# Kernel optimization log

Measured on AMD Instinct MI355X. Metric: run time of the kernel, lower is better.

## Reference

```python
import jax, jax.numpy as jnp
import numpy as np

C = 128   # channels / dim
NH = 4    # num heads
HD = C // NH
K = 5     # conv kernel size: t=int((log2(128)+1)/2)=4 -> k=5
P = 12    # patch size
GH = 8    # grid height/width (96/12)
NPATCH = GH * GH
FEAT = P * P * C


def _ln(x, g, b):
    m = jnp.mean(x, -1, keepdims=True)
    v = jnp.var(x, -1, keepdims=True)
    return (x - m) / jnp.sqrt(v + 1e-5) * g + b


def _conv1d(x, w, pad):
    return jax.lax.conv_general_dilated(x, w, (1,), [(pad, pad)], dimension_numbers=('NCH', 'OIH', 'NCH'))


def _pool(x, out):
    # exact adaptive avg pool when H % out == 0
    B, c, H, W = x.shape
    f = H // out
    return x.reshape(B, c, out, f, out, f).mean((3, 5))


def _bilinear_ac(x, out):
    # bilinear interpolate [B,C,H,H] -> [B,C,out,out], align_corners=True
    H = x.shape[2]
    cpos = jnp.arange(out) * (H - 1) / (out - 1)
    i0 = jnp.floor(cpos).astype(jnp.int32)
    i1 = jnp.minimum(i0 + 1, H - 1)
    w = (cpos - i0).astype(x.dtype)
    xh = x[:, :, i0, :] * (1 - w)[None, None, :, None] + x[:, :, i1, :] * w[None, None, :, None]
    return xh[:, :, :, i0] * (1 - w) + xh[:, :, :, i1] * w


def setup_inputs() -> dict:
    key = jax.random.key(0)
    ks = jax.random.split(key, 8)
    B = 16
    return {
        's1': jax.random.normal(ks[0], (B, C, 96, 96), jnp.float32),
        'o': jax.random.normal(ks[1], (B, C, 64, 64), jnp.float32),
        'index': jax.random.randint(ks[2], (4, 2), 0, 96),
        'pe_w': jax.random.normal(ks[3], (64, 64, K), jnp.float32) * 0.05,
        'bn_g': jnp.ones((64,), jnp.float32),
        'bn_b': jnp.zeros((64,), jnp.float32),
        'bn_m': jnp.zeros((64,), jnp.float32),
        'bn_v': jnp.ones((64,), jnp.float32),
        'lnx_g': jnp.ones((C,), jnp.float32),
        'lnx_b': jnp.zeros((C,), jnp.float32),
        'lny_g': jnp.ones((C,), jnp.float32),
        'lny_b': jnp.zeros((C,), jnp.float32),
        'qkv_w': jax.random.normal(ks[4], (3 * C, C), jnp.float32) * 0.02,
        'qkv_b': jnp.zeros((3 * C,), jnp.float32),
        'yv_w': jax.random.normal(ks[5], (C, C), jnp.float32) * 0.02,
        'yv_b': jnp.zeros((C,), jnp.float32),
        'proj_w': jax.random.normal(ks[6], (C, C), jnp.float32) * 0.02,
        'proj_b': jnp.zeros((C,), jnp.float32),
        'c1d_w': jax.random.normal(ks[7], (C, C, K), jnp.float32) * 0.05,
    }


def reference(s1, o, index, pe_w, bn_g, bn_b, bn_m, bn_v, lnx_g, lnx_b, lny_g, lny_b,
              qkv_w, qkv_b, yv_w, yv_b, proj_w, proj_b, c1d_w):
    B = s1.shape[0]
    pad = (K - 1) // 2
    # --- mask(s1): patch embedding, conv1d+BN(eval)+ReLU, selective-square mask ---
    # einops: b c (h p1) (w p2) -> b (h w) (p1 p2 c)
    x = s1.reshape(B, C, GH, P, GH, P).transpose(0, 2, 4, 3, 5, 1).reshape(B, NPATCH, FEAT)
    x = _conv1d(x, pe_w, pad)
    x = (x - bn_m[None, :, None]) / jnp.sqrt(bn_v + 1e-5)[None, :, None] * bn_g[None, :, None] + bn_b[None, :, None]
    x = jax.nn.relu(x)
    # mask: rows at center indices keep value (mul by 1), all other rows squared
    idxs = index[:, 0] // P * GH + index[:, 1] // P
    sel = jnp.zeros((NPATCH,), bool).at[idxs].set(True)
    x = x * jnp.where(sel[None, :, None], 1.0, x)
    # einops back: b (h w) (p1 p2 c) -> b c (h p1) (w p2), then pool to 32
    x = x.reshape(B, GH, GH, P, P, C).transpose(0, 5, 1, 3, 2, 4).reshape(B, C, 96, 96)
    short = _pool(x, 32)                                   # [B,C,32,32]
    # --- attention branch ---
    op = _pool(o, 32)
    N = 32 * 32
    of = _ln(op.reshape(B, C, N).transpose(0, 2, 1), lnx_g, lnx_b)   # [B,N,C]
    ori = short.reshape(B, C, N).transpose(0, 2, 1)
    sn = _ln(ori, lny_g, lny_b)
    qkv = (of @ qkv_w.T + qkv_b).reshape(B, N, 3, NH, HD).transpose(2, 0, 3, 1, 4)
    q, k, v = qkv[0], qkv[1], qkv[2]                       # each [B,H,N,D]
    yv = (sn @ yv_w.T + yv_b).reshape(B, N, NH, HD).transpose(0, 2, 1, 3)
    attn = jax.nn.softmax(jnp.einsum('bhnd,bhmd->bhnm', q, k) * HD ** -0.5, axis=-1)
    xv = v + jnp.einsum('bhnm,bhmd->bhnd', attn, yv)
    xv = xv.transpose(0, 2, 1, 3).reshape(B, N, C) @ proj_w.T + proj_b
    xv = (xv + ori).transpose(0, 2, 1)                     # [B,C,N]
    xv = xv + _conv1d(xv, c1d_w, pad)
    xv = xv.reshape(B, C, 32, 32)
    return _bilinear_ac(xv, 96)
```

## Files before the change

kernel.cpp:

```cpp
#include <hip/hip_runtime.h>

#define FEAT 18432

typedef __attribute__((ext_vector_type(8))) short short8;
typedef __attribute__((ext_vector_type(4))) float f32x4;

__device__ __forceinline__ float b2f(unsigned short s) {
  union { unsigned int u; float f; } v; v.u = ((unsigned int)s) << 16; return v.f;
}
__device__ __forceinline__ unsigned short f2bf(float x) {
  union { float f; unsigned int u; } v; v.f = x;
  unsigned int u = v.u;
  unsigned int r = (u + 0x7FFFu + ((u >> 16) & 1u)) >> 16;
  return (unsigned short)r;
}

__device__ __forceinline__ void gl_lds16(const void* g, void* l) {
  __builtin_amdgcn_global_load_lds(
      (const __attribute__((address_space(1))) unsigned int*)g,
      (__attribute__((address_space(3))) unsigned int*)l, 16, 0, 0);
}

__global__ __launch_bounds__(256) void k_transpose(const float* __restrict__ s1,
                                                   unsigned short* __restrict__ xT) {
  int c = blockIdx.x, b = blockIdx.y;
  __shared__ float lds[96 * 99];
  int t = threadIdx.x;
  const float* src = s1 + ((size_t)b * 128 + c) * 9216;
  for (int idx = t; idx < 2304; idx += 256) {
    float4 v = ((const float4*)src)[idx];
    int h = idx / 24, w0 = (idx - h * 24) * 4;
    float* p = lds + h * 99 + w0;
    p[0] = v.x; p[1] = v.y; p[2] = v.z; p[3] = v.w;
  }
  __syncthreads();
  unsigned short* dstb = xT + (size_t)b * FEAT * 64;
  int sw = c & 7;
  for (int idx = t; idx < 1152; idx += 256) {
    int p1p2 = idx >> 3, gh = idx & 7;
    int p1 = p1p2 / 12, p2 = p1p2 - p1 * 12;
    const float* row = lds + (gh * 12 + p1) * 99 + p2;
    uint4 u;
    u.x = f2bf(row[0])  | ((unsigned int)f2bf(row[12]) << 16);
    u.y = f2bf(row[24]) | ((unsigned int)f2bf(row[36]) << 16);
    u.z = f2bf(row[48]) | ((unsigned int)f2bf(row[60]) << 16);
    u.w = f2bf(row[72]) | ((unsigned int)f2bf(row[84]) << 16);
    int f = p1p2 * 128 + c;
    int pos = gh ^ sw;
    *(uint4*)(dstb + (size_t)f * 64 + pos * 8) = u;
  }
}

__global__ __launch_bounds__(256) void k_prep(const float* __restrict__ pe_w,
                                              unsigned short* __restrict__ wpk) {
  int oc0 = blockIdx.x * 8;
  for (int e = threadIdx.x; e < 2560; e += 256) {
    int oc = oc0 + e / 320;
    int kL = e - (e / 320) * 320;
    int ic = kL & 63, kk = kL >> 6;
    float v = pe_w[(oc * 64 + ic) * 5 + kk];
    int LC = kL >> 3;
    int pos = (LC & 56) | ((LC & 7) ^ (oc & 7));
    wpk[oc * 320 + (pos << 3) + (kL & 7)] = f2bf(v);
  }
}

__global__ __launch_bounds__(256) void k_prepc(const float* __restrict__ cw,
                                               float* __restrict__ cwt) {
  int e0 = (blockIdx.x * 256 + threadIdx.x) * 4;
#pragma unroll
  for (int j = 0; j < 4; ++j) {
    int e = e0 + j;
    int r = e >> 7, oc = e & 127;
    cwt[e] = cw[(size_t)oc * 640 + r];
  }
}

__global__ __launch_bounds__(256) void k_prepw(const float* __restrict__ W,
                                               unsigned short* __restrict__ dst,
                                               int ncols) {
  int idx = blockIdx.x * 256 + threadIdx.x;
  if (idx >= ncols * 16) return;
  int n = idx >> 4, c = idx & 15;
  int slot = (c & 8) | ((c & 7) ^ (n & 7));
  const float* s = W + (size_t)n * 128 + c * 8;
  uint4 u;
  u.x = (unsigned int)f2bf(s[0]) | ((unsigned int)f2bf(s[1]) << 16);
  u.y = (unsigned int)f2bf(s[2]) | ((unsigned int)f2bf(s[3]) << 16);
  u.z = (unsigned int)f2bf(s[4]) | ((unsigned int)f2bf(s[5]) << 16);
  u.w = (unsigned int)f2bf(s[6]) | ((unsigned int)f2bf(s[7]) << 16);
  *(uint4*)(dst + (size_t)n * 128 + slot * 8) = u;
}

__global__ __launch_bounds__(256) void k_conv_pe(
    const unsigned short* __restrict__ xT, const unsigned short* __restrict__ wpk,
    const float* __restrict__ bn_g, const float* __restrict__ bn_b,
    const float* __restrict__ bn_m, const float* __restrict__ bn_v,
    const int* __restrict__ indexp, unsigned short* __restrict__ ym) {
  extern __shared__ char smem[];
  unsigned short* Wl = (unsigned short*)smem;
  unsigned short* xl = (unsigned short*)(smem + 40960);
  float* scf = (float*)(smem + 74240);
  float* shf = (float*)(smem + 74496);
  int*   sli = (int*)(smem + 74752);
  int t = threadIdx.x;
  int b = blockIdx.y;
  int blk_f0 = blockIdx.x << 9;
  int lane = t & 63, w = t >> 6;
  int n16 = lane & 15, q = lane >> 4;

  for (int j = 0; j < 10; ++j) {
    int seg = w * 10 + j;
    gl_lds16((const char*)wpk + (seg << 10) + lane * 16, (char*)Wl + (seg << 10));
  }
  if (t < 64) {
    float sc = bn_g[t] * rsqrtf(bn_v[t] + 1e-5f);
    scf[t] = sc;
    shf[t] = bn_b[t] - bn_m[t] * sc;
    int i0 = indexp[0] / 12 * 8 + indexp[1] / 12;
    int i1 = indexp[2] / 12 * 8 + indexp[3] / 12;
    int i2 = indexp[4] / 12 * 8 + indexp[5] / 12;
    int i3 = indexp[6] / 12 * 8 + indexp[7] / 12;
    sli[t] = (t == i0 || t == i1 || t == i2 || t == i3) ? 1 : 0;
  }

  const unsigned short* xb = xT + (size_t)b * FEAT * 64;
  const unsigned int* xbu = (const unsigned int*)xb;

  for (int wnd = 0; wnd < 2; ++wnd) {
    int F0 = blk_f0 + (wnd << 8);
    __syncthreads();
    int flA = (F0 == 0) ? 2 : 0;
    for (int j = 0; j < 8; ++j) {
      int seg = (w << 3) + j;
      int gRow = F0 - 2 + flA + (seg << 3);
      gl_lds16((const char*)xb + (size_t)gRow * 128 + lane * 16,
               (char*)xl + flA * 128 + (seg << 10));
    }
    if (t < 128) {
      int r0 = (flA == 2) ? 0 : 256;
      int fl = (t < 64) ? (r0 + (t >> 5)) : (258 + ((t >> 5) & 1));
      int j = t & 31;
      int f = F0 - 2 + fl;
      unsigned int v = 0;
      if (f >= 0 && f < FEAT) v = xbu[(size_t)f * 32 + j];
      ((unsigned int*)xl)[fl * 32 + j] = v;
    }
    __syncthreads();

    f32x4 acc[4][4];
#pragma unroll
    for (int mt = 0; mt < 4; ++mt)
#pragma unroll
      for (int nt = 0; nt < 4; ++nt) acc[mt][nt] = (f32x4){0.f, 0.f, 0.f, 0.f};

    int rowB = w * 64 + n16;
#pragma unroll
    for (int kk = 0; kk < 5; ++kk) {
      int swb = (n16 + kk + 6) & 7;
#pragma unroll
      for (int ih = 0; ih < 2; ++ih) {
        int ca = (ih << 2) | q;
        const unsigned short* Ap = Wl + kk * 64 + ((ca ^ (n16 & 7)) << 3) + n16 * 320;
        short8 a0 = *(const short8*)(Ap);
        short8 a1 = *(const short8*)(Ap + 16 * 320);
        short8 a2 = *(const short8*)(Ap + 32 * 320);
        short8 a3 = *(const short8*)(Ap + 48 * 320);
        const unsigned short* Bp = xl + ((ca ^ swb) << 3) + (rowB + kk) * 64;
        short8 b0 = *(const short8*)(Bp);
        short8 b1 = *(const short8*)(Bp + 16 * 64);
        short8 b2 = *(const short8*)(Bp + 32 * 64);
        short8 b3 = *(const short8*)(Bp + 48 * 64);
        acc[0][0] = __builtin_amdgcn_mfma_f32_16x16x32_bf16(a0, b0, acc[0][0], 0, 0, 0);
        acc[0][1] = __builtin_amdgcn_mfma_f32_16x16x32_bf16(a0, b1, acc[0][1], 0, 0, 0);
        acc[0][2] = __builtin_amdgcn_mfma_f32_16x16x32_bf16(a0, b2, acc[0][2], 0, 0, 0);
        acc[0][3] = __builtin_amdgcn_mfma_f32_16x16x32_bf16(a0, b3, acc[0][3], 0, 0, 0);
        acc[1][0] = __builtin_amdgcn_mfma_f32_16x16x32_bf16(a1, b0, acc[1][0], 0, 0, 0);
        acc[1][1] = __builtin_amdgcn_mfma_f32_16x16x32_bf16(a1, b1, acc[1][1], 0, 0, 0);
        acc[1][2] = __builtin_amdgcn_mfma_f32_16x16x32_bf16(a1, b2, acc[1][2], 0, 0, 0);
        acc[1][3] = __builtin_amdgcn_mfma_f32_16x16x32_bf16(a1, b3, acc[1][3], 0, 0, 0);
        acc[2][0] = __builtin_amdgcn_mfma_f32_16x16x32_bf16(a2, b0, acc[2][0], 0, 0, 0);
        acc[2][1] = __builtin_amdgcn_mfma_f32_16x16x32_bf16(a2, b1, acc[2][1], 0, 0, 0);
        acc[2][2] = __builtin_amdgcn_mfma_f32_16x16x32_bf16(a2, b2, acc[2][2], 0, 0, 0);
        acc[2][3] = __builtin_amdgcn_mfma_f32_16x16x32_bf16(a2, b3, acc[2][3], 0, 0, 0);
        acc[3][0] = __builtin_amdgcn_mfma_f32_16x16x32_bf16(a3, b0, acc[3][0], 0, 0, 0);
        acc[3][1] = __builtin_amdgcn_mfma_f32_16x16x32_bf16(a3, b1, acc[3][1], 0, 0, 0);
        acc[3][2] = __builtin_amdgcn_mfma_f32_16x16x32_bf16(a3, b2, acc[3][2], 0, 0, 0);
        acc[3][3] = __builtin_amdgcn_mfma_f32_16x16x32_bf16(a3, b3, acc[3][3], 0, 0, 0);
      }
    }

#pragma unroll
    for (int mt = 0; mt < 4; ++mt) {
#pragma unroll
      for (int i = 0; i < 4; ++i) {
        int oc = mt * 16 + q * 4 + i;
        float sc = scf[oc], sh = shf[oc];
        bool sel = sli[oc] != 0;
        unsigned short* yo = ym + ((size_t)b * 64 + oc) * FEAT + F0 + w * 64 + n16;
#pragma unroll
        for (int nt = 0; nt < 4; ++nt) {
          float y = fmaf(acc[mt][nt][i], sc, sh);
          y = fmaxf(y, 0.f);
          if (!sel) y *= y;
          yo[nt * 16] = f2bf(y);
        }
      }
    }
  }
}

__global__ __launch_bounds__(256) void k_pool9ln(
    const unsigned short* __restrict__ ym, const float* __restrict__ lng,
    const float* __restrict__ lnb, float* __restrict__ ori,
    unsigned short* __restrict__ snh) {
  int oc = blockIdx.x, b = blockIdx.y;
  const unsigned short* src = ym + ((size_t)b * 64 + oc) * FEAT;
  int oh0 = (oc >> 3) << 2, ow0 = (oc & 7) << 2;
  __shared__ float red[8];
  int t = threadIdx.x;
  int c = t & 127, hr = t >> 7, wv = t >> 6, l64 = t & 63;
  float g = lng[c], bb = lnb[c];
  for (int p = 0; p < 8; ++p) {
    int nl = p * 2 + hr;
    int pg1 = nl >> 2, pg2 = nl & 3;
    int pbase = (pg1 * 36 + pg2 * 3) * 128 + c;
    float s = 0.f;
#pragma unroll
    for (int dy = 0; dy < 3; ++dy)
#pragma unroll
      for (int dx = 0; dx < 3; ++dx)
        s += b2f(src[pbase + (dy * 12 + dx) * 128]);
    float val = s * (1.f / 9.f);
    float su = val, q = val * val;
#pragma unroll
    for (int off = 32; off > 0; off >>= 1) {
      su += __shfl_xor(su, off, 64);
      q += __shfl_xor(q, off, 64);
    }
    if (l64 == 0) { red[wv * 2] = su; red[wv * 2 + 1] = q; }
    __syncthreads();
    float S = red[hr * 4 + 0] + red[hr * 4 + 2];
    float Q = red[hr * 4 + 1] + red[hr * 4 + 3];
    float mean = S * (1.f / 128.f);
    float var = Q * (1.f / 128.f) - mean * mean;
    float inv = rsqrtf(var + 1e-5f);
    int n = (oh0 + pg1) * 32 + ow0 + pg2;
    size_t base = ((size_t)b * 1024 + n) * 128;
    ori[base + c] = val;
    float lnv = (val - mean) * inv * g + bb;
    int ch = c >> 3;
    int slot = (ch & 8) | ((ch & 7) ^ (n & 7));
    snh[base + slot * 8 + (c & 7)] = f2bf(lnv);
    __syncthreads();
  }
}

__global__ __launch_bounds__(256) void k_poolo_ln(
    const float* __restrict__ o, const float* __restrict__ lng,
    const float* __restrict__ lnb, unsigned short* __restrict__ oflh) {
  int y = blockIdx.x, b = blockIdx.y;
  __shared__ float pl[128 * 33];
  int t = threadIdx.x;
  for (int idx = t; idx < 4096; idx += 256) {
    int xo = idx & 31, c = idx >> 5;
    const float* p = o + (((size_t)b * 128 + c) * 64 + 2 * y) * 64 + 2 * xo;
    float2 a = *(const float2*)p;
    float2 d = *(const float2*)(p + 64);
    pl[c * 33 + xo] = 0.25f * (a.x + a.y + d.x + d.y);
  }
  __syncthreads();
  int xo = t >> 3, l8 = t & 7;
  float v[16]; float s = 0.f, q = 0.f;
#pragma unroll
  for (int i = 0; i < 16; ++i) {
    float x = pl[(l8 * 16 + i) * 33 + xo];
    v[i] = x; s += x; q += x * x;
  }
#pragma unroll
  for (int off = 1; off < 8; off <<= 1) {
    s += __shfl_xor(s, off, 8);
    q += __shfl_xor(q, off, 8);
  }
  float mean = s * (1.f / 128.f);
  float var = q * (1.f / 128.f) - mean * mean;
  float inv = rsqrtf(var + 1e-5f);
  int n = y * 32 + xo;
  unsigned short* dst = oflh + ((size_t)b * 1024 + n) * 128;
  int m7 = n & 7;
#pragma unroll
  for (int h = 0; h < 2; ++h) {
    int c = l8 * 2 + h;
    int slot = (c & 8) | ((c & 7) ^ m7);
    uint4 u;
    float w0 = (v[h * 8 + 0] - mean) * inv * lng[c * 8 + 0] + lnb[c * 8 + 0];
    float w1 = (v[h * 8 + 1] - mean) * inv * lng[c * 8 + 1] + lnb[c * 8 + 1];
    float w2 = (v[h * 8 + 2] - mean) * inv * lng[c * 8 + 2] + lnb[c * 8 + 2];
    float w3 = (v[h * 8 + 3] - mean) * inv * lng[c * 8 + 3] + lnb[c * 8 + 3];
    float w4 = (v[h * 8 + 4] - mean) * inv * lng[c * 8 + 4] + lnb[c * 8 + 4];
    float w5 = (v[h * 8 + 5] - mean) * inv * lng[c * 8 + 5] + lnb[c * 8 + 5];
    float w6 = (v[h * 8 + 6] - mean) * inv * lng[c * 8 + 6] + lnb[c * 8 + 6];
    float w7 = (v[h * 8 + 7] - mean) * inv * lng[c * 8 + 7] + lnb[c * 8 + 7];
    u.x = (unsigned int)f2bf(w0) | ((unsigned int)f2bf(w1) << 16);
    u.y = (unsigned int)f2bf(w2) | ((unsigned int)f2bf(w3) << 16);
    u.z = (unsigned int)f2bf(w4) | ((unsigned int)f2bf(w5) << 16);
    u.w = (unsigned int)f2bf(w6) | ((unsigned int)f2bf(w7) << 16);
    *(uint4*)(dst + slot * 8) = u;
  }
}

__global__ __launch_bounds__(256) void k_gemm_mfma(
    const unsigned short* __restrict__ A, const unsigned short* __restrict__ W,
    const float* __restrict__ bias, float* __restrict__ out, int Ncols) {
  __shared__ unsigned short Al[128 * 128];
  __shared__ unsigned short Bl[64 * 128];
  int m0 = blockIdx.x << 7, n0 = blockIdx.y << 6;
  int t = threadIdx.x;
  int lane = t & 63, w = t >> 6;
  int n16 = lane & 15, q = lane >> 4;

  for (int j = 0; j < 8; ++j) {
    int seg = w * 8 + j;
    gl_lds16((const char*)A + (size_t)m0 * 256 + (seg << 10) + lane * 16,
             (char*)Al + (seg << 10));
  }
  for (int j = 0; j < 4; ++j) {
    int seg = w * 4 + j;
    gl_lds16((const char*)W + (size_t)n0 * 256 + (seg << 10) + lane * 16,
             (char*)Bl + (seg << 10));
  }
  __syncthreads();

  int wm = w >> 1, wn = w & 1;
  f32x4 acc[4][2];
#pragma unroll
  for (int mt = 0; mt < 4; ++mt)
#pragma unroll
    for (int nt = 0; nt < 2; ++nt) acc[mt][nt] = (f32x4){0.f, 0.f, 0.f, 0.f};

#pragma unroll
  for (int kf = 0; kf < 4; ++kf) {
    int ca = kf * 4 + q;
    int rA0 = wm * 64 + n16;
    const unsigned short* Ap0 = Al + (size_t)rA0 * 128;
    int slotA = (ca & 8) | ((ca & 7) ^ (rA0 & 7));
    short8 a0 = *(const short8*)(Ap0 + slotA * 8);
    short8 a1 = *(const short8*)(Ap0 + 16 * 128 + slotA * 8);
    short8 a2 = *(const short8*)(Ap0 + 32 * 128 + slotA * 8);
    short8 a3 = *(const short8*)(Ap0 + 48 * 128 + slotA * 8);
    int rB0 = wn * 32 + n16;
    const unsigned short* Bp0 = Bl + (size_t)rB0 * 128;
    int slotB = (ca & 8) | ((ca & 7) ^ (rB0 & 7));
    short8 b0 = *(const short8*)(Bp0 + slotB * 8);
    short8 b1 = *(const short8*)(Bp0 + 16 * 128 + slotB * 8);
    acc[0][0] = __builtin_amdgcn_mfma_f32_16x16x32_bf16(a0, b0, acc[0][0], 0, 0, 0);
    acc[0][1] = __builtin_amdgcn_mfma_f32_16x16x32_bf16(a0, b1, acc[0][1], 0, 0, 0);
    acc[1][0] = __builtin_amdgcn_mfma_f32_16x16x32_bf16(a1, b0, acc[1][0], 0, 0, 0);
    acc[1][1] = __builtin_amdgcn_mfma_f32_16x16x32_bf16(a1, b1, acc[1][1], 0, 0, 0);
    acc[2][0] = __builtin_amdgcn_mfma_f32_16x16x32_bf16(a2, b0, acc[2][0], 0, 0, 0);
    acc[2][1] = __builtin_amdgcn_mfma_f32_16x16x32_bf16(a2, b1, acc[2][1], 0, 0, 0);
    acc[3][0] = __builtin_amdgcn_mfma_f32_16x16x32_bf16(a3, b0, acc[3][0], 0, 0, 0);
    acc[3][1] = __builtin_amdgcn_mfma_f32_16x16x32_bf16(a3, b1, acc[3][1], 0, 0, 0);
  }

#pragma unroll
  for (int mt = 0; mt < 4; ++mt) {
#pragma unroll
    for (int i = 0; i < 4; ++i) {
      int m = m0 + wm * 64 + mt * 16 + q * 4 + i;
#pragma unroll
      for (int nt = 0; nt < 2; ++nt) {
        int n = n0 + wn * 32 + nt * 16 + n16;
        out[(size_t)m * Ncols + n] = acc[mt][nt][i] + bias[n];
      }
    }
  }
}

__global__ __launch_bounds__(256) void k_proj_mfma(
    const unsigned short* __restrict__ A, const unsigned short* __restrict__ W,
    const float* __restrict__ bias, const float* __restrict__ ori,
    float* __restrict__ xv2) {
  __shared__ unsigned short Al[128 * 128];
  __shared__ unsigned short Bl[64 * 128];
  int m0 = blockIdx.x << 7, n0 = blockIdx.y << 6;
  int t = threadIdx.x;
  int lane = t & 63, w = t >> 6;
  int n16 = lane & 15, q = lane >> 4;

  for (int j = 0; j < 8; ++j) {
    int seg = w * 8 + j;
    gl_lds16((const char*)A + (size_t)m0 * 256 + (seg << 10) + lane * 16,
             (char*)Al + (seg << 10));
  }
  for (int j = 0; j < 4; ++j) {
    int seg = w * 4 + j;
    gl_lds16((const char*)W + (size_t)n0 * 256 + (seg << 10) + lane * 16,
             (char*)Bl + (seg << 10));
  }
  __syncthreads();

  int wm = w >> 1, wn = w & 1;
  f32x4 acc[4][2];
#pragma unroll
  for (int mt = 0; mt < 4; ++mt)
#pragma unroll
    for (int nt = 0; nt < 2; ++nt) acc[mt][nt] = (f32x4){0.f, 0.f, 0.f, 0.f};

#pragma unroll
  for (int kf = 0; kf < 4; ++kf) {
    int ca = kf * 4 + q;
    int rA0 = wm * 64 + n16;
    const unsigned short* Ap0 = Al + (size_t)rA0 * 128;
    int slotA = (ca & 8) | ((ca & 7) ^ (rA0 & 7));
    short8 a0 = *(const short8*)(Ap0 + slotA * 8);
    short8 a1 = *(const short8*)(Ap0 + 16 * 128 + slotA * 8);
    short8 a2 = *(const short8*)(Ap0 + 32 * 128 + slotA * 8);
    short8 a3 = *(const short8*)(Ap0 + 48 * 128 + slotA * 8);
    int rB0 = wn * 32 + n16;
    const unsigned short* Bp0 = Bl + (size_t)rB0 * 128;
    int slotB = (ca & 8) | ((ca & 7) ^ (rB0 & 7));
    short8 b0 = *(const short8*)(Bp0 + slotB * 8);
    short8 b1 = *(const short8*)(Bp0 + 16 * 128 + slotB * 8);
    acc[0][0] = __builtin_amdgcn_mfma_f32_16x16x32_bf16(a0, b0, acc[0][0], 0, 0, 0);
    acc[0][1] = __builtin_amdgcn_mfma_f32_16x16x32_bf16(a0, b1, acc[0][1], 0, 0, 0);
    acc[1][0] = __builtin_amdgcn_mfma_f32_16x16x32_bf16(a1, b0, acc[1][0], 0, 0, 0);
    acc[1][1] = __builtin_amdgcn_mfma_f32_16x16x32_bf16(a1, b1, acc[1][1], 0, 0, 0);
    acc[2][0] = __builtin_amdgcn_mfma_f32_16x16x32_bf16(a2, b0, acc[2][0], 0, 0, 0);
    acc[2][1] = __builtin_amdgcn_mfma_f32_16x16x32_bf16(a2, b1, acc[2][1], 0, 0, 0);
    acc[3][0] = __builtin_amdgcn_mfma_f32_16x16x32_bf16(a3, b0, acc[3][0], 0, 0, 0);
    acc[3][1] = __builtin_amdgcn_mfma_f32_16x16x32_bf16(a3, b1, acc[3][1], 0, 0, 0);
  }

  int bb = m0 >> 10;
  int nbase = (m0 & 1023) + wm * 64;
#pragma unroll
  for (int mt = 0; mt < 4; ++mt) {
    int nloc = nbase + mt * 16 + q * 4;
    const float* orow = ori + ((size_t)bb * 1024 + nloc) * 128;
#pragma unroll
    for (int nt = 0; nt < 2; ++nt) {
      int c = n0 + wn * 32 + nt * 16 + n16;
      float pb = bias[c];
      float4 vv;
      vv.x = acc[mt][nt][0] + pb + orow[c];
      vv.y = acc[mt][nt][1] + pb + orow[128 + c];
      vv.z = acc[mt][nt][2] + pb + orow[256 + c];
      vv.w = acc[mt][nt][3] + pb + orow[384 + c];
      *(float4*)(xv2 + ((size_t)bb * 128 + c) * 1024 + nloc) = vv;
    }
  }
}

__global__ __launch_bounds__(256) void k_cvt(const float* __restrict__ qkv,
                                             const float* __restrict__ yv,
                                             unsigned short* __restrict__ qkb,
                                             unsigned short* __restrict__ vtb) {
  int nt = blockIdx.x, b = blockIdx.y;
  int n0 = nt << 6;
  int t = threadIdx.x;
  __shared__ unsigned short tl[64 * 132];
  const float* qb = qkv + ((size_t)b * 1024 + n0) * 384;
  for (int it = 0; it < 16; ++it) {
    int idx = it * 256 + t;
    int n = idx >> 6, c4 = idx & 63;
    float4 v = *(const float4*)(qb + (size_t)n * 384 + c4 * 4);
    int c = c4 << 2;
    int kind = c >> 7, h = (c >> 5) & 3, d = c & 31;
    uint2 u;
    u.x = (unsigned int)f2bf(v.x) | ((unsigned int)f2bf(v.y) << 16);
    u.y = (unsigned int)f2bf(v.z) | ((unsigned int)f2bf(v.w) << 16);
    *(uint2*)(qkb + ((((size_t)b * 4 + h) * 2 + kind) * 1024 + n0 + n) * 32 + d) = u;
  }
  const float* vb = yv + ((size_t)b * 1024 + n0) * 128;
  for (int it = 0; it < 8; ++it) {
    int idx = it * 256 + t;
    int n = idx >> 5, c4 = idx & 31;
    float4 v = *(const float4*)(vb + (size_t)n * 128 + c4 * 4);
    unsigned short* o = tl + n * 132 + c4 * 4;
    o[0] = f2bf(v.x); o[1] = f2bf(v.y); o[2] = f2bf(v.z); o[3] = f2bf(v.w);
  }
  __syncthreads();
  int c = t >> 1, half = t & 1;
  unsigned short* orow = vtb + (((size_t)b * 4 + (c >> 5)) * 32 + (c & 31)) * 1024 + n0 + half * 32;
#pragma unroll
  for (int k = 0; k < 4; ++k) {
    short8 pack;
#pragma unroll
    for (int j = 0; j < 8; ++j)
      pack[j] = (short)tl[(half * 32 + k * 8 + j) * 132 + c];
    *(short8*)(orow + k * 8) = pack;
  }
}

__global__ __launch_bounds__(256) void k_attn(const float* __restrict__ qkv,
                                              const unsigned short* __restrict__ qkb,
                                              const unsigned short* __restrict__ vtb,
                                              unsigned short* __restrict__ atth) {
  int qt = blockIdx.x, h = blockIdx.y, b = blockIdx.z;
  __shared__ unsigned short Qs[64 * 40];
  __shared__ unsigned short Ks[64 * 40];
  __shared__ unsigned short Vt[32 * 72];
  __shared__ unsigned short Pw[4 * 16 * 68];
  int t = threadIdx.x;
  int lane = t & 63, w = t >> 6;
  int quad = lane >> 4, l16 = lane & 15;
  const float* qbase = qkv + (size_t)b * 1024 * 384;
  const unsigned short* qrow = qkb + (((size_t)b * 4 + h) * 2 + 0) * 1024 * 32;
  const unsigned short* krow = qkb + (((size_t)b * 4 + h) * 2 + 1) * 1024 * 32;
  const unsigned short* vrow = vtb + ((size_t)b * 4 + h) * 32 * 1024;
  int q0 = qt << 6;
  int hd = h * 32;

  {
    int r = t >> 2, cq = t & 3;
    short8 v = *(const short8*)(qrow + (size_t)(q0 + r) * 32 + cq * 8);
    *(short8*)(Qs + r * 40 + cq * 8) = v;
  }
  __syncthreads();
  short8 aq = *(const short8*)(Qs + (w * 16 + l16) * 40 + quad * 8);

  f32x4 O[2];
  O[0] = (f32x4){0.f, 0.f, 0.f, 0.f};
  O[1] = (f32x4){0.f, 0.f, 0.f, 0.f};
  float mi0 = -1e30f, li0 = 0.f;
  unsigned short* Pme = Pw + w * (16 * 68);
  const float scl = 0.17677669529663688f;

  for (int ci = 0; ci < 16; ++ci) {
    __syncthreads();
    int kn0 = ci << 6;
    {
      int r = t >> 2, cq = t & 3;
      short8 kv = *(const short8*)(krow + (size_t)(kn0 + r) * 32 + cq * 8);
      *(short8*)(Ks + r * 40 + cq * 8) = kv;
      int d = t >> 3, cc = t & 7;
      short8 vv = *(const short8*)(vrow + (size_t)d * 1024 + kn0 + cc * 8);
      *(short8*)(Vt + d * 72 + cc * 8) = vv;
    }
    __syncthreads();

    f32x4 S[4];
#pragma unroll
    for (int nt = 0; nt < 4; ++nt) S[nt] = (f32x4){0.f, 0.f, 0.f, 0.f};
#pragma unroll
    for (int nt = 0; nt < 4; ++nt) {
      short8 bk = *(const short8*)(Ks + (nt * 16 + l16) * 40 + quad * 8);
      S[nt] = __builtin_amdgcn_mfma_f32_16x16x32_bf16(bk, aq, S[nt], 0, 0, 0);
    }

    float sv[16];
#pragma unroll
    for (int nt = 0; nt < 4; ++nt)
#pragma unroll
      for (int r = 0; r < 4; ++r) sv[nt * 4 + r] = S[nt][r] * scl;
    float m0 = fmaxf(fmaxf(sv[0], sv[1]), fmaxf(sv[2], sv[3]));
    float m1 = fmaxf(fmaxf(sv[4], sv[5]), fmaxf(sv[6], sv[7]));
    float m2 = fmaxf(fmaxf(sv[8], sv[9]), fmaxf(sv[10], sv[11]));
    float m3 = fmaxf(fmaxf(sv[12], sv[13]), fmaxf(sv[14], sv[15]));
    float rm = fmaxf(fmaxf(m0, m1), fmaxf(m2, m3));
    rm = fmaxf(rm, __shfl_xor(rm, 16));
    rm = fmaxf(rm, __shfl_xor(rm, 32));
    float nm = fmaxf(mi0, rm);
    float alpha = __expf(mi0 - nm);
    mi0 = nm;

    float psnt[4];
    unsigned short* pwr = Pme + l16 * 68 + quad * 4;
#pragma unroll
    for (int nt = 0; nt < 4; ++nt) {
      float p0 = __expf(sv[nt * 4 + 0] - nm);
      float p1 = __expf(sv[nt * 4 + 1] - nm);
      float p2 = __expf(sv[nt * 4 + 2] - nm);
      float p3 = __expf(sv[nt * 4 + 3] - nm);
      psnt[nt] = (p0 + p1) + (p2 + p3);
      uint2 u;
      u.x = (unsigned int)f2bf(p0) | ((unsigned int)f2bf(p1) << 16);
      u.y = (unsigned int)f2bf(p2) | ((unsigned int)f2bf(p3) << 16);
      *(uint2*)(pwr + nt * 16) = u;
    }
    float ps = (psnt[0] + psnt[1]) + (psnt[2] + psnt[3]);
    ps += __shfl_xor(ps, 16);
    ps += __shfl_xor(ps, 32);
    li0 = li0 * alpha + ps;

    float al0 = __shfl(alpha, quad * 4 + 0);
    float al1 = __shfl(alpha, quad * 4 + 1);
    float al2 = __shfl(alpha, quad * 4 + 2);
    float al3 = __shfl(alpha, quad * 4 + 3);
    O[0][0] *= al0; O[1][0] *= al0;
    O[0][1] *= al1; O[1][1] *= al1;
    O[0][2] *= al2; O[1][2] *= al2;
    O[0][3] *= al3; O[1][3] *= al3;

#pragma unroll
    for (int kc = 0; kc < 2; ++kc) {
      short8 bv0 = *(const short8*)(Vt + l16 * 72 + kc * 32 + quad * 8);
      short8 bv1 = *(const short8*)(Vt + (16 + l16) * 72 + kc * 32 + quad * 8);
      short8 ap = *(const short8*)(Pme + l16 * 68 + kc * 32 + quad * 8);
      O[0] = __builtin_amdgcn_mfma_f32_16x16x32_bf16(ap, bv0, O[0], 0, 0, 0);
      O[1] = __builtin_amdgcn_mfma_f32_16x16x32_bf16(ap, bv1, O[1], 0, 0, 0);
    }
  }

#pragma unroll
  for (int reg = 0; reg < 4; ++reg) {
    float lit = __shfl(li0, quad * 4 + reg);
    int n = q0 + w * 16 + quad * 4 + reg;
    float inv = 1.f / lit;
    size_t mrow = ((size_t)b * 1024 + n) * 128;
    int m7 = n & 7;
#pragma unroll
    for (int nt = 0; nt < 2; ++nt) {
      int dd = hd + nt * 16 + l16;
      float val = O[nt][reg] * inv + qbase[(size_t)n * 384 + 256 + dd];
      int ch = dd >> 3;
      int slot = (ch & 8) | ((ch & 7) ^ m7);
      atth[mrow + slot * 8 + (dd & 7)] = f2bf(val);
    }
  }
}

__global__ __launch_bounds__(256) void k_conv1d(
    const float* __restrict__ xv2, const float* __restrict__ cwt,
    float* __restrict__ xv3) {
  extern __shared__ char cs[];
  float* xl = (float*)cs;
  float* wl = (float*)(cs + 18432);
  int nt = blockIdx.x, b = blockIdx.y;
  int n0 = nt << 5;
  int t = threadIdx.x;
  int lane = t & 63, w = t >> 6;
  const float* xb = xv2 + (size_t)b * 128 * 1024;
  for (int idx = t; idx < 4608; idx += 256) {
    int ic = idx / 36, j = idx - ic * 36;
    int n = n0 + j - 2;
    xl[idx] = (n >= 0 && n < 1024) ? xb[(size_t)ic * 1024 + n] : 0.f;
  }

  int oc = t & 127, g = t >> 7;
  float acc[16];
#pragma unroll
  for (int i = 0; i < 16; ++i) acc[i] = 0.f;

#pragma unroll 1
  for (int ch = 0; ch < 16; ++ch) {
    __syncthreads();
#pragma unroll
    for (int j = 0; j < 5; ++j) {
      int seg = w * 5 + j;
      gl_lds16((const char*)cwt + (size_t)ch * 20480 + (seg << 10) + lane * 16,
               (char*)wl + (seg << 10));
    }
    __syncthreads();

#pragma unroll
    for (int icl = 0; icl < 8; ++icl) {
      int ic = ch * 8 + icl;
      const float* xr = xl + ic * 36 + (g << 4);
      float xw[20];
#pragma unroll
      for (int q2 = 0; q2 < 5; ++q2) {
        float4 v = *(const float4*)(xr + q2 * 4);
        xw[q2 * 4] = v.x; xw[q2 * 4 + 1] = v.y; xw[q2 * 4 + 2] = v.z; xw[q2 * 4 + 3] = v.w;
      }
      const float* wr = wl + icl * 5 * 128 + oc;
      float w0 = wr[0], w1 = wr[128], w2 = wr[256], w3 = wr[384], w4 = wr[512];
#pragma unroll
      for (int i = 0; i < 16; ++i)
        acc[i] = fmaf(xw[i], w0, fmaf(xw[i + 1], w1, fmaf(xw[i + 2], w2,
                 fmaf(xw[i + 3], w3, fmaf(xw[i + 4], w4, acc[i])))));
    }
  }

  const float* res = xb + (size_t)oc * 1024 + n0 + (g << 4);
  float* outp = xv3 + ((size_t)b * 128 + oc) * 1024 + n0 + (g << 4);
#pragma unroll
  for (int q2 = 0; q2 < 4; ++q2) {
    float4 r = *(const float4*)(res + q2 * 4);
    float4 o_;
    o_.x = r.x + acc[q2 * 4 + 0];
    o_.y = r.y + acc[q2 * 4 + 1];
    o_.z = r.z + acc[q2 * 4 + 2];
    o_.w = r.w + acc[q2 * 4 + 3];
    *(float4*)(outp + q2 * 4) = o_;
  }
}

__global__ __launch_bounds__(256) void k_bilinear(const float* __restrict__ xv3,
                                                  float* __restrict__ out) {
  int idx = blockIdx.x * 256 + threadIdx.x;
  int X = idx % 96;
  int t2 = idx / 96;
  int Y = t2 % 96;
  int bc = t2 / 96;
  const float* src = xv3 + (size_t)bc * 1024;
  const float r = 31.f / 95.f;
  float py = Y * r, px = X * r;
  int y0 = (int)py, x0 = (int)px;
  float wy = py - y0, wx = px - x0;
  int y1 = y0 < 31 ? y0 + 1 : 31, x1 = x0 < 31 ? x0 + 1 : 31;
  float a = src[y0 * 32 + x0], b_ = src[y0 * 32 + x1];
  float c_ = src[y1 * 32 + x0], d_ = src[y1 * 32 + x1];
  float t0 = a * (1.f - wy) + c_ * wy;
  float t1 = b_ * (1.f - wy) + d_ * wy;
  out[idx] = t0 * (1.f - wx) + t1 * wx;
}

extern "C" void kernel_launch(void* const* d_in, const int* in_sizes, int n_in,
                              void* d_out, int out_size, void* d_ws, size_t ws_size,
                              hipStream_t stream) {
  (void)in_sizes; (void)n_in; (void)out_size; (void)ws_size;
  const float* s1    = (const float*)d_in[0];
  const float* o     = (const float*)d_in[1];
  const int*   indx  = (const int*)d_in[2];
  const float* pe_w  = (const float*)d_in[3];
  const float* bn_g  = (const float*)d_in[4];
  const float* bn_b  = (const float*)d_in[5];
  const float* bn_m  = (const float*)d_in[6];
  const float* bn_v  = (const float*)d_in[7];
  const float* lnx_g = (const float*)d_in[8];
  const float* lnx_b = (const float*)d_in[9];
  const float* lny_g = (const float*)d_in[10];
  const float* lny_b = (const float*)d_in[11];
  const float* qkv_w = (const float*)d_in[12];
  const float* qkv_b = (const float*)d_in[13];
  const float* yv_w  = (const float*)d_in[14];
  const float* yv_b  = (const float*)d_in[15];
  const float* proj_w = (const float*)d_in[16];
  const float* proj_b = (const float*)d_in[17];
  const float* c1d_w  = (const float*)d_in[18];

  char* ws = (char*)d_ws;
  unsigned short* xTh = (unsigned short*)ws;
  unsigned short* ymh = (unsigned short*)(ws + 37748736);
  unsigned short* wpk = (unsigned short*)d_out;
  float* cwt = (float*)((char*)d_out + 65536);
  unsigned short* wqkh = (unsigned short*)((char*)d_out + 458752);
  unsigned short* wyvh = (unsigned short*)((char*)d_out + 573440);
  unsigned short* wprh = (unsigned short*)((char*)d_out + 622592);
  float* ori  = (float*)ws;
  unsigned short* snh  = (unsigned short*)(ws + 8388608);
  unsigned short* oflh = (unsigned short*)(ws + 16777216);
  unsigned short* atth = (unsigned short*)(ws + 25165824);
  float* qkvb  = (float*)(ws + 37748736);
  float* yvbuf = (float*)(ws + 62914560);
  unsigned short* qkb = (unsigned short*)(ws + 16777216);
  unsigned short* vtb = (unsigned short*)(ws + 71303168);
  float* xv2   = (float*)(ws + 37748736);
  float* xv3   = (float*)(ws + 46137344);

  hipLaunchKernelGGL(k_prep, dim3(8), dim3(256), 0, stream, pe_w, wpk);
  hipLaunchKernelGGL(k_prepc, dim3(80), dim3(256), 0, stream, c1d_w, cwt);
  hipLaunchKernelGGL(k_prepw, dim3(24), dim3(256), 0, stream, qkv_w, wqkh, 384);
  hipLaunchKernelGGL(k_prepw, dim3(8), dim3(256), 0, stream, yv_w, wyvh, 128);
  hipLaunchKernelGGL(k_prepw, dim3(8), dim3(256), 0, stream, proj_w, wprh, 128);
  hipLaunchKernelGGL(k_transpose, dim3(128, 16), dim3(256), 0, stream, s1, xTh);
  hipLaunchKernelGGL(k_conv_pe, dim3(36, 16), dim3(256), 75008, stream,
                     xTh, wpk, bn_g, bn_b, bn_m, bn_v, indx, ymh);
  hipLaunchKernelGGL(k_pool9ln, dim3(64, 16), dim3(256), 0, stream, ymh, lny_g, lny_b, ori, snh);
  hipLaunchKernelGGL(k_poolo_ln, dim3(32, 16), dim3(256), 0, stream, o, lnx_g, lnx_b, oflh);
  hipLaunchKernelGGL(k_gemm_mfma, dim3(128, 6), dim3(256), 0, stream, oflh, wqkh, qkv_b, qkvb, 384);
  hipLaunchKernelGGL(k_gemm_mfma, dim3(128, 2), dim3(256), 0, stream, snh, wyvh, yv_b, yvbuf, 128);
  hipLaunchKernelGGL(k_cvt, dim3(16, 16), dim3(256), 0, stream, qkvb, yvbuf, qkb, vtb);
  hipLaunchKernelGGL(k_attn, dim3(16, 4, 16), dim3(256), 0, stream, qkvb, qkb, vtb, atth);
  hipLaunchKernelGGL(k_proj_mfma, dim3(128, 2), dim3(256), 0, stream, atth, wprh, proj_b, ori, xv2);
  hipLaunchKernelGGL(k_conv1d, dim3(32, 16), dim3(256), 38912, stream, xv2, cwt, xv3);
  hipLaunchKernelGGL(k_bilinear, dim3(73728), dim3(256), 0, stream, xv3, (float*)d_out);
}
```

Before: 393.6 us.

## Run channel conv1d as bf16 MFMA GEMM with swizzled LDS tiles

Replaces the scalar FP32 conv1d over channels with an MFMA bf16 implicit GEMM. The weights are prepacked into a swizzled bf16 layout, and the projection kernel also emits a bf16 position-major copy of its output that serves as the conv input. The goal is to move the 128x640 per-position contraction off the FP32 FMA pipes onto matrix cores. In exchange it adds an extra bf16 write in proj and uses bf16 precision for the conv operands.

```diff
diff --git a/kernel.cpp b/kernel.cpp
--- a/kernel.cpp
+++ b/kernel.cpp
@@ -65,15 +65,15 @@
   }
 }
 
-__global__ __launch_bounds__(256) void k_prepc(const float* __restrict__ cw,
-                                               float* __restrict__ cwt) {
-  int e0 = (blockIdx.x * 256 + threadIdx.x) * 4;
-#pragma unroll
-  for (int j = 0; j < 4; ++j) {
-    int e = e0 + j;
-    int r = e >> 7, oc = e & 127;
-    cwt[e] = cw[(size_t)oc * 640 + r];
-  }
+__global__ __launch_bounds__(256) void k_prepcw(const float* __restrict__ cw,
+                                                unsigned short* __restrict__ wch) {
+  int e = blockIdx.x * 256 + threadIdx.x;
+  int oc = e / 640, kl = e - (e / 640) * 640;
+  int kk = kl >> 7, ic = kl & 127;
+  float v = cw[(size_t)oc * 640 + ic * 5 + kk];
+  int LC = kl >> 3;
+  int pos = (LC & 120) | ((LC & 7) ^ (oc & 7));
+  wch[(size_t)oc * 640 + pos * 8 + (kl & 7)] = f2bf(v);
 }
 
 __global__ __launch_bounds__(256) void k_prepw(const float* __restrict__ W,
@@ -380,7 +380,7 @@
 __global__ __launch_bounds__(256) void k_proj_mfma(
     const unsigned short* __restrict__ A, const unsigned short* __restrict__ W,
     const float* __restrict__ bias, const float* __restrict__ ori,
-    float* __restrict__ xv2) {
+    float* __restrict__ xv2, unsigned short* __restrict__ xph) {
   __shared__ unsigned short Al[128 * 128];
   __shared__ unsigned short Bl[64 * 128];
   int m0 = blockIdx.x << 7, n0 = blockIdx.y << 6;
@@ -448,6 +448,14 @@
       vv.z = acc[mt][nt][2] + pb + orow[256 + c];
       vv.w = acc[mt][nt][3] + pb + orow[384 + c];
       *(float4*)(xv2 + ((size_t)bb * 128 + c) * 1024 + nloc) = vv;
+      int ch = c >> 3, ce = c & 7;
+#pragma unroll
+      for (int i = 0; i < 4; ++i) {
+        int nrow = nloc + i;
+        int slot = (ch & 8) | ((ch & 7) ^ (nrow & 7));
+        float val = (i == 0) ? vv.x : (i == 1) ? vv.y : (i == 2) ? vv.z : vv.w;
+        xph[((size_t)bb * 1024 + nrow) * 128 + slot * 8 + ce] = f2bf(val);
+      }
     }
   }
 }
@@ -621,69 +629,86 @@
   }
 }
 
-__global__ __launch_bounds__(256) void k_conv1d(
-    const float* __restrict__ xv2, const float* __restrict__ cwt,
-    float* __restrict__ xv3) {
+__global__ __launch_bounds__(256) void k_conv1d_mfma(
+    const unsigned short* __restrict__ xph, const unsigned short* __restrict__ wch,
+    const float* __restrict__ xv2, float* __restrict__ xv3) {
   extern __shared__ char cs[];
-  float* xl = (float*)cs;
-  float* wl = (float*)(cs + 18432);
-  int nt = blockIdx.x, b = blockIdx.y;
-  int n0 = nt << 5;
-  int t = threadIdx.x;
-  int lane = t & 63, w = t >> 6;
-  const float* xb = xv2 + (size_t)b * 128 * 1024;
-  for (int idx = t; idx < 4608; idx += 256) {
-    int ic = idx / 36, j = idx - ic * 36;
+  unsigned short* Wl = (unsigned short*)cs;
+  unsigned short* xl = (unsigned short*)(cs + 81920);
+  int ntile = blockIdx.x, b = blockIdx.y, oh = blockIdx.z;
+  int n0 = ntile << 7;
+  int t = threadIdx.x, lane = t & 63, w = t >> 6;
+  int n16 = lane & 15, q = lane >> 4;
+
+  const unsigned short* wsrc = wch + (size_t)oh * 64 * 640;
+  for (int j = 0; j < 20; ++j) {
+    int seg = w * 20 + j;
+    gl_lds16((const char*)wsrc + (seg << 10) + lane * 16, (char*)Wl + (seg << 10));
+  }
+  const unsigned short* xpb = xph + (size_t)b * 1024 * 128;
+  for (int j = 0; j < 8; ++j) {
+    int seg = w * 8 + j;
+    gl_lds16((const char*)xpb + (size_t)n0 * 256 + (seg << 10) + lane * 16,
+             (char*)xl + 512 + (seg << 10));
+  }
+  {
+    int ri = t >> 6, j2 = t & 63;
+    int j = (ri < 2) ? ri : (128 + ri);
     int n = n0 + j - 2;
-    xl[idx] = (n >= 0 && n < 1024) ? xb[(size_t)ic * 1024 + n] : 0.f;
-  }
-
-  int oc = t & 127, g = t >> 7;
-  float acc[16];
-#pragma unroll
-  for (int i = 0; i < 16; ++i) acc[i] = 0.f;
-
-#pragma unroll 1
-  for (int ch = 0; ch < 16; ++ch) {
-    __syncthreads();
-#pragma unroll
-    for (int j = 0; j < 5; ++j) {
-      int seg = w * 5 + j;
-      gl_lds16((const char*)cwt + (size_t)ch * 20480 + (seg << 10) + lane * 16,
-               (char*)wl + (seg << 10));
-    }
-    __syncthreads();
-
-#pragma unroll
-    for (int icl = 0; icl < 8; ++icl) {
-      int ic = ch * 8 + icl;
-      const float* xr = xl + ic * 36 + (g << 4);
-      float xw[20];
-#pragma unroll
-      for (int q2 = 0; q2 < 5; ++q2) {
-        float4 v = *(const float4*)(xr + q2 * 4);
-        xw[q2 * 4] = v.x; xw[q2 * 4 + 1] = v.y; xw[q2 * 4 + 2] = v.z; xw[q2 * 4 + 3] = v.w;
+    unsigned int v = 0;
+    if (n >= 0 && n < 1024) v = ((const unsigned int*)xpb)[(size_t)n * 64 + j2];
+    ((unsigned int*)xl)[j * 64 + j2] = v;
+  }
+  __syncthreads();
+
+  f32x4 acc[4][2];
+#pragma unroll
+  for (int mt = 0; mt < 4; ++mt)
+#pragma unroll
+    for (int nt = 0; nt < 2; ++nt) acc[mt][nt] = (f32x4){0.f, 0.f, 0.f, 0.f};
+
+  int nb = w * 32;
+#pragma unroll
+  for (int kk = 0; kk < 5; ++kk) {
+    int swb = (n16 + kk + 6) & 7;
+#pragma unroll
+    for (int kf = 0; kf < 4; ++kf) {
+      int ca = kf * 4 + q;
+      int LC = kk * 16 + kf * 4 + q;
+      int slotA = (LC & 120) | ((LC & 7) ^ (n16 & 7));
+      const unsigned short* Ap = Wl + n16 * 640 + slotA * 8;
+      short8 a0 = *(const short8*)(Ap);
+      short8 a1 = *(const short8*)(Ap + 16 * 640);
+      short8 a2 = *(const short8*)(Ap + 32 * 640);
+      short8 a3 = *(const short8*)(Ap + 48 * 640);
+      int slotB = (ca & 8) | ((ca & 7) ^ swb);
+      const unsigned short* Bp = xl + (nb + n16 + kk) * 128 + slotB * 8;
+      short8 b0 = *(const short8*)(Bp);
+      short8 b1 = *(const short8*)(Bp + 16 * 128);
+      acc[0][0] = __builtin_amdgcn_mfma_f32_16x16x32_bf16(a0, b0, acc[0][0], 0, 0, 0);
+      acc[0][1] = __builtin_amdgcn_mfma_f32_16x16x32_bf16(a0, b1, acc[0][1], 0, 0, 0);
+      acc[1][0] = __builtin_amdgcn_mfma_f32_16x16x32_bf16(a1, b0, acc[1][0], 0, 0, 0);
+      acc[1][1] = __builtin_amdgcn_mfma_f32_16x16x32_bf16(a1, b1, acc[1][1], 0, 0, 0);
+      acc[2][0] = __builtin_amdgcn_mfma_f32_16x16x32_bf16(a2, b0, acc[2][0], 0, 0, 0);
+      acc[2][1] = __builtin_amdgcn_mfma_f32_16x16x32_bf16(a2, b1, acc[2][1], 0, 0, 0);
+      acc[3][0] = __builtin_amdgcn_mfma_f32_16x16x32_bf16(a3, b0, acc[3][0], 0, 0, 0);
+      acc[3][1] = __builtin_amdgcn_mfma_f32_16x16x32_bf16(a3, b1, acc[3][1], 0, 0, 0);
+    }
+  }
+
+#pragma unroll
+  for (int mt = 0; mt < 4; ++mt) {
+#pragma unroll
+    for (int i = 0; i < 4; ++i) {
+      int oc = oh * 64 + mt * 16 + q * 4 + i;
+      const float* res = xv2 + ((size_t)b * 128 + oc) * 1024;
+      float* outp = xv3 + ((size_t)b * 128 + oc) * 1024;
+#pragma unroll
+      for (int nt = 0; nt < 2; ++nt) {
+        int n = n0 + nb + nt * 16 + n16;
+        outp[n] = acc[mt][nt][i] + res[n];
       }
-      const float* wr = wl + icl * 5 * 128 + oc;
-      float w0 = wr[0], w1 = wr[128], w2 = wr[256], w3 = wr[384], w4 = wr[512];
-#pragma unroll
-      for (int i = 0; i < 16; ++i)
-        acc[i] = fmaf(xw[i], w0, fmaf(xw[i + 1], w1, fmaf(xw[i + 2], w2,
-                 fmaf(xw[i + 3], w3, fmaf(xw[i + 4], w4, acc[i])))));
-    }
-  }
-
-  const float* res = xb + (size_t)oc * 1024 + n0 + (g << 4);
-  float* outp = xv3 + ((size_t)b * 128 + oc) * 1024 + n0 + (g << 4);
-#pragma unroll
-  for (int q2 = 0; q2 < 4; ++q2) {
-    float4 r = *(const float4*)(res + q2 * 4);
-    float4 o_;
-    o_.x = r.x + acc[q2 * 4 + 0];
-    o_.y = r.y + acc[q2 * 4 + 1];
-    o_.z = r.z + acc[q2 * 4 + 2];
-    o_.w = r.w + acc[q2 * 4 + 3];
-    *(float4*)(outp + q2 * 4) = o_;
+    }
   }
 }
 
@@ -735,7 +760,7 @@
   unsigned short* xTh = (unsigned short*)ws;
   unsigned short* ymh = (unsigned short*)(ws + 37748736);
   unsigned short* wpk = (unsigned short*)d_out;
-  float* cwt = (float*)((char*)d_out + 65536);
+  unsigned short* wch = (unsigned short*)((char*)d_out + 65536);
   unsigned short* wqkh = (unsigned short*)((char*)d_out + 458752);
   unsigned short* wyvh = (unsigned short*)((char*)d_out + 573440);
   unsigned short* wprh = (unsigned short*)((char*)d_out + 622592);
@@ -749,9 +774,10 @@
   unsigned short* vtb = (unsigned short*)(ws + 71303168);
   float* xv2   = (float*)(ws + 37748736);
   float* xv3   = (float*)(ws + 46137344);
+  unsigned short* xph = (unsigned short*)(ws + 62914560);
 
   hipLaunchKernelGGL(k_prep, dim3(8), dim3(256), 0, stream, pe_w, wpk);
-  hipLaunchKernelGGL(k_prepc, dim3(80), dim3(256), 0, stream, c1d_w, cwt);
+  hipLaunchKernelGGL(k_prepcw, dim3(320), dim3(256), 0, stream, c1d_w, wch);
   hipLaunchKernelGGL(k_prepw, dim3(24), dim3(256), 0, stream, qkv_w, wqkh, 384);
   hipLaunchKernelGGL(k_prepw, dim3(8), dim3(256), 0, stream, yv_w, wyvh, 128);
   hipLaunchKernelGGL(k_prepw, dim3(8), dim3(256), 0, stream, proj_w, wprh, 128);
@@ -764,7 +790,7 @@
   hipLaunchKernelGGL(k_gemm_mfma, dim3(128, 2), dim3(256), 0, stream, snh, wyvh, yv_b, yvbuf, 128);
   hipLaunchKernelGGL(k_cvt, dim3(16, 16), dim3(256), 0, stream, qkvb, yvbuf, qkb, vtb);
   hipLaunchKernelGGL(k_attn, dim3(16, 4, 16), dim3(256), 0, stream, qkvb, qkb, vtb, atth);
-  hipLaunchKernelGGL(k_proj_mfma, dim3(128, 2), dim3(256), 0, stream, atth, wprh, proj_b, ori, xv2);
-  hipLaunchKernelGGL(k_conv1d, dim3(32, 16), dim3(256), 38912, stream, xv2, cwt, xv3);
+  hipLaunchKernelGGL(k_proj_mfma, dim3(128, 2), dim3(256), 0, stream, atth, wprh, proj_b, ori, xv2, xph);
+  hipLaunchKernelGGL(k_conv1d_mfma, dim3(8, 16, 2), dim3(256), 115712, stream, xph, wch, xv2, xv3);
   hipLaunchKernelGGL(k_bilinear, dim3(73728), dim3(256), 0, stream, xv3, (float*)d_out);
 }
```

New measurement: 355.4 us. 9.7% less time.
